# Optimization experiments

Measured on AMD Instinct MI355X. Metric: run time of the kernel, lower is better.

The kernel has to match this reference:

```python
import jax, jax.numpy as jnp
import numpy as np

B, T, C = 4, 2048, 1024
H = 16
D = C // H  # head_dim = 64


def setup_inputs() -> dict:
    key = jax.random.key(0)
    k1, k2, k3 = jax.random.split(key, 3)
    x = jax.random.normal(k1, (B, T, C), dtype=jnp.float32)
    # torch nn.Linear weight layout: [out_features, in_features]; y = x @ W.T
    w_attn = jax.random.normal(k2, (3 * C, C), dtype=jnp.float32) * (1.0 / np.sqrt(C))
    w_proj = jax.random.normal(k3, (C, C), dtype=jnp.float32) * (1.0 / np.sqrt(C))
    return {"x": x, "w_attn": w_attn, "w_proj": w_proj}


def _attention(x, w_attn, w_proj):
    qkv = jnp.einsum('btc,fc->btf', x, w_attn)           # [B,T,3C]
    q, k, v = jnp.split(qkv, 3, axis=-1)
    # [B,T,C] -> [B,H,T,D]
    q = q.reshape(B, T, H, D).transpose(0, 2, 1, 3)
    k = k.reshape(B, T, H, D).transpose(0, 2, 1, 3)
    v = v.reshape(B, T, H, D).transpose(0, 2, 1, 3)
    att = jnp.einsum('bhqd,bhkd->bhqk', q, k) * (1.0 / np.sqrt(D))
    causal = jnp.tril(jnp.ones((T, T), dtype=bool))      # [T,T]
    att = jnp.where(causal[None, None], att, -jnp.inf)
    att = jax.nn.softmax(att, axis=-1)
    out = jnp.einsum('bhqk,bhkd->bhqd', att, v)          # [B,H,T,D]
    out = out.transpose(0, 2, 1, 3).reshape(B, T, C)
    return jnp.einsum('btc,fc->btf', out, w_proj)        # [B,T,C]


def reference(x, w_attn, w_proj):
    return _attention(x, w_attn, w_proj)
```

## Files before the change

kernel.cpp:

```cpp
#include <hip/hip_runtime.h>
#include <hip/hip_bf16.h>

typedef __attribute__((ext_vector_type(8))) short s8b;
typedef __attribute__((ext_vector_type(4))) float f4;
typedef unsigned short u16;

union U8 { s8b v; unsigned long long u[2]; };

__device__ __forceinline__ u16 f2bf(float f) {
  union { float f; unsigned u; } x; x.f = f;
  unsigned r = x.u + 0x7fffu + ((x.u >> 16) & 1u);
  return (u16)(r >> 16);
}

__device__ __forceinline__ float exp2a(float x) {
  float r;
  asm("v_exp_f32 %0, %1" : "=v"(r) : "v"(x));
  return r;
}

__device__ __forceinline__ void gload16(const void* g, void* l) {
  __builtin_amdgcn_global_load_lds(
      (const __attribute__((address_space(1))) void*)g,
      (__attribute__((address_space(3))) void*)l, 16, 0, 0);
}

__global__ void cvt3_kernel(const float* __restrict__ x, const float* __restrict__ wa,
                            const float* __restrict__ wp, u16* __restrict__ xb,
                            u16* __restrict__ wab, u16* __restrict__ wpb) {
  const int i = blockIdx.x * blockDim.x + threadIdx.x;
  const float4* src;
  ushort4* dst;
  int idx;
  if (i < 2097152) { src = (const float4*)x; dst = (ushort4*)xb; idx = i; }
  else if (i < 2883584) { src = (const float4*)wa; dst = (ushort4*)wab; idx = i - 2097152; }
  else { src = (const float4*)wp; dst = (ushort4*)wpb; idx = i - 2883584; }
  const float4 v = src[idx];
  ushort4 o;
  o.x = f2bf(v.x); o.y = f2bf(v.y); o.z = f2bf(v.z); o.w = f2bf(v.w);
  dst[idx] = o;
}

#define BMT 128
#define BNT 128
#define BKT 64

template<int MODE, int TILES>
__global__ __launch_bounds__(256, 2)
void gemm_bt(const u16* __restrict__ A, const u16* __restrict__ Bm,
             float* __restrict__ Cf,
             u16* __restrict__ qo, u16* __restrict__ ko, u16* __restrict__ vo,
             int N, int K, int GX) {
  __shared__ u16 lds[2][2][BMT * BKT];
  const int tid = threadIdx.x;
  const int lane = tid & 63;
  const int w = tid >> 6;
  const int wr = w >> 1, wc = w & 1;
  const int ric = lane >> 3;
  const int ssw = (lane & 7) ^ ric;

  auto tile_ptrs = [&](int t, const u16*& Ab, const u16*& Bb, int& bm, int& bn) {
    const int d = blockIdx.x + t * gridDim.x;
    const int xcd = d & 7, ib = d >> 3;
    bm = xcd * 8 + ib / GX;
    bn = ib % GX;
    Ab = A + (size_t)bm * BMT * K;
    Bb = Bm + (size_t)bn * BNT * K;
  };

  const int nk = K / BKT;
  const u16 *Ab, *Bb, *AbN, *BbN;
  int bm, bn, bmN, bnN;
  tile_ptrs(0, Ab, Bb, bm, bn);

  {
#pragma unroll
    for (int c = 0; c < 4; ++c) {
      const int rch = w * 32 + c * 8;
      gload16(Ab + (size_t)(rch + ric) * K + ssw * 8, &lds[0][0][rch * BKT]);
      gload16(Bb + (size_t)(rch + ric) * K + ssw * 8, &lds[0][1][rch * BKT]);
    }
  }
  __syncthreads();

  for (int t = 0; t < TILES; ++t) {
    if (t + 1 < TILES) tile_ptrs(t + 1, AbN, BbN, bmN, bnN);
    f4 acc[4][4] = {};

    for (int kt = 0; kt < nk; kt += 2) {
#pragma unroll
      for (int h = 0; h < 2; ++h) {
        const int ktg = kt + h;
        {
          const u16* sA;
          const u16* sB;
          int ko_;
          bool do_stage = true;
          if (ktg + 1 < nk) { sA = Ab; sB = Bb; ko_ = (ktg + 1) * BKT; }
          else if (t + 1 < TILES) { sA = AbN; sB = BbN; ko_ = 0; }
          else do_stage = false;
          if (do_stage) {
#pragma unroll
            for (int c = 0; c < 4; ++c) {
              const int rch = w * 32 + c * 8;
              gload16(sA + (size_t)(rch + ric) * K + ko_ + ssw * 8, &lds[h ^ 1][0][rch * BKT]);
              gload16(sB + (size_t)(rch + ric) * K + ko_ + ssw * 8, &lds[h ^ 1][1][rch * BKT]);
            }
          }
        }
        const u16* At = &lds[h][0][0];
        const u16* Bt = &lds[h][1][0];
#pragma unroll
        for (int kk = 0; kk < 2; ++kk) {
          s8b a[4], b[4];
#pragma unroll
          for (int m = 0; m < 4; ++m) {
            const int row = wr * 64 + m * 16 + (lane & 15);
            a[m] = *(const s8b*)(At + row * BKT + ((((kk << 2) + (lane >> 4)) ^ (row & 7)) << 3));
          }
#pragma unroll
          for (int n = 0; n < 4; ++n) {
            const int row = wc * 64 + n * 16 + (lane & 15);
            b[n] = *(const s8b*)(Bt + row * BKT + ((((kk << 2) + (lane >> 4)) ^ (row & 7)) << 3));
          }
#pragma unroll
          for (int m = 0; m < 4; ++m)
#pragma unroll
            for (int n = 0; n < 4; ++n)
              acc[m][n] = __builtin_amdgcn_mfma_f32_16x16x32_bf16(a[m], b[n], acc[m][n], 0, 0, 0);
        }
        __syncthreads();
      }
    }

    if (MODE == 0) {
#pragma unroll
      for (int n = 0; n < 4; ++n) {
        const int f = bn * BNT + wc * 64 + n * 16 + (lane & 15);
        const int which = f >> 10;
        const int rem = f & 1023;
        const int h = rem >> 6, dd = rem & 63;
        if (which == 2) {
#pragma unroll
          for (int m = 0; m < 4; ++m) {
            const int i0 = bm * BMT + wr * 64 + m * 16 + (lane >> 4) * 4;
            const int bb = i0 >> 11, t0 = i0 & 2047;
            ushort4 pk;
            pk.x = f2bf(acc[m][n][0]);
            pk.y = f2bf(acc[m][n][1]);
            pk.z = f2bf(acc[m][n][2]);
            pk.w = f2bf(acc[m][n][3]);
            *(ushort4*)(&vo[((size_t)((bb << 4) + h) * 64 + dd) * 2048 + t0]) = pk;
          }
        } else {
          u16* dst = which == 0 ? qo : ko;
          const float sc = which == 0 ? 0.18033688f : 1.0f;
#pragma unroll
          for (int m = 0; m < 4; ++m) {
#pragma unroll
            for (int j = 0; j < 4; ++j) {
              const int i = bm * BMT + wr * 64 + m * 16 + (lane >> 4) * 4 + j;
              const int bb = i >> 11, tt = i & 2047;
              dst[((size_t)((bb << 4) + h) * 2048 + tt) * 64 + dd] = f2bf(acc[m][n][j] * sc);
            }
          }
        }
      }
    } else {
#pragma unroll
      for (int m = 0; m < 4; ++m) {
#pragma unroll
        for (int j = 0; j < 4; ++j) {
          const int i = bm * BMT + wr * 64 + m * 16 + (lane >> 4) * 4 + j;
#pragma unroll
          for (int n = 0; n < 4; ++n) {
            const int f = bn * BNT + wc * 64 + n * 16 + (lane & 15);
            Cf[(size_t)i * N + f] = acc[m][n][j];
          }
        }
      }
    }

    Ab = AbN; Bb = BbN; bm = bmN; bn = bnN;
  }
}

__global__ __launch_bounds__(256, 3)
void attn_kernel(const u16* __restrict__ q, const u16* __restrict__ k,
                 const u16* __restrict__ vt, u16* __restrict__ ao) {
  __shared__ u16 Kl[2][64 * 64];
  __shared__ u16 VTl[2][64 * 64];
  __shared__ u16 Pl[4][16 * 64];
  const int tid = threadIdx.x, lane = tid & 63, w = tid >> 6;
  const int dd = blockIdx.x;
  const int xcd = dd & 7, ib = dd >> 3;
  const int bh = xcd * 8 + (ib & 7);
  const int j4 = ib >> 3;
  const int s4 = j4 >> 2, r4 = j4 & 3;
  const int qi = (s4 == 0) ? 15 - r4 : (s4 == 1) ? 8 + r4 : (s4 == 2) ? 7 - r4 : r4;
  const int b = bh >> 4, h16 = bh & 15;
  const size_t hb = (size_t)bh * 2048 * 64;
  const int qlo = lane & 15, hi = lane >> 4;
  const int r0 = tid >> 3, sl = tid & 7;
  u16* pw = &Pl[w][0];

  const s8b ones = {16256, 16256, 16256, 16256, 16256, 16256, 16256, 16256};

  const u16* kp = k + hb + (size_t)r0 * 64 + sl * 8;
  const u16* vp = vt + hb + (size_t)r0 * 2048 + sl * 8;
  s8b kr[2], vr[2];
  auto load_regs = [&]() {
    kr[0] = *(const s8b*)kp;
    kr[1] = *(const s8b*)(kp + 32 * 64);
    vr[0] = *(const s8b*)vp;
    vr[1] = *(const s8b*)(vp + 32 * 2048);
    kp += 64 * 64;
    vp += 64;
  };

  auto softpack = [&](f4 (&s)[4], U8 (&pf)[2]) {
#pragma unroll
    for (int n = 0; n < 4; ++n)
#pragma unroll
      for (int j = 0; j < 4; ++j) s[n][j] = exp2a(s[n][j]);
#pragma unroll
    for (int n = 0; n < 4; ++n) {
      __hip_bfloat162 h0 = __float22bfloat162_rn(make_float2(s[n][0], s[n][1]));
      __hip_bfloat162 h1 = __float22bfloat162_rn(make_float2(s[n][2], s[n][3]));
      unsigned lo, hi2;
      __builtin_memcpy(&lo, &h0, 4);
      __builtin_memcpy(&hi2, &h1, 4);
      const unsigned long long w64 =
          (unsigned long long)lo | ((unsigned long long)hi2 << 32);
      const int cw = ((n << 2) + hi) ^ qlo;
      *(unsigned long long*)(pw + (qlo << 6) + (cw << 2)) = w64;
    }
#pragma unroll
    for (int kk = 0; kk < 2; ++kk) {
      const int ca = ((kk << 3) + (hi << 1)) ^ qlo;
      pf[kk].u[0] = *(const unsigned long long*)(pw + (qlo << 6) + (ca << 2));
      pf[kk].u[1] = *(const unsigned long long*)(pw + (qlo << 6) + ((ca ^ 1) << 2));
    }
  };

  const int nkt = 2 * qi + 2;
  s8b qf[2][2];
#pragma unroll
  for (int g = 0; g < 2; ++g) {
    const u16* qp = q + hb + (size_t)(qi * 128 + w * 32 + g * 16 + qlo) * 64 + hi * 8;
    qf[g][0] = *(const s8b*)qp;
    qf[g][1] = *(const s8b*)(qp + 32);
  }
  f4 acc0[5] = {}, acc1[5] = {};

  load_regs();
  {
#pragma unroll
    for (int c0 = 0; c0 < 2; ++c0) {
      const int r = r0 + c0 * 32;
      const int off = r * 64 + ((sl ^ (r & 7) ^ (r >> 3)) << 3);
      *(s8b*)(&Kl[0][off]) = kr[c0];
      *(s8b*)(&VTl[0][off]) = vr[c0];
    }
  }
  __syncthreads();

  for (int kt2 = 0; kt2 < nkt; kt2 += 2) {
#pragma unroll
    for (int h = 0; h < 2; ++h) {
      const int ktg = kt2 + h;
      const bool pf_next = (ktg + 1 < nkt);
      if (pf_next) load_regs();

      f4 s0[4], s1[4];
#pragma unroll
      for (int n = 0; n < 4; ++n) {
        s0[n] = (f4){-64.f, -64.f, -64.f, -64.f};
        s1[n] = (f4){-64.f, -64.f, -64.f, -64.f};
      }
      __builtin_amdgcn_s_setprio(1);
#pragma unroll
      for (int n = 0; n < 4; ++n) {
        const int row = n * 16 + qlo;
        const int swz = (row & 7) ^ (row >> 3);
#pragma unroll
        for (int kk = 0; kk < 2; ++kk) {
          const s8b kf = *(const s8b*)(&Kl[h][row * 64 + ((((kk << 2) + hi) ^ swz) << 3)]);
          s0[n] = __builtin_amdgcn_mfma_f32_16x16x32_bf16(kf, qf[0][kk], s0[n], 0, 0, 0);
          s1[n] = __builtin_amdgcn_mfma_f32_16x16x32_bf16(kf, qf[1][kk], s1[n], 0, 0, 0);
        }
      }
      __builtin_amdgcn_s_setprio(0);

      const int dmb = (2 * qi - ktg) * 64;
      if (dmb < 64) {
        const int thr0 = w * 32 + qlo + dmb;
        const int thr1 = thr0 + 16;
#pragma unroll
        for (int n = 0; n < 4; ++n)
#pragma unroll
          for (int j = 0; j < 4; ++j) {
            const int kidx = n * 16 + hi * 4 + j;
            if (kidx > thr0) s0[n][j] = -1e30f;
            if (kidx > thr1) s1[n][j] = -1e30f;
          }
      }

      U8 pf0[2], pf1[2];
      softpack(s0, pf0);
      softpack(s1, pf1);

      __builtin_amdgcn_s_setprio(1);
#pragma unroll
      for (int dn = 0; dn < 4; ++dn) {
        const int vrow = dn * 16 + qlo;
        const int vswz = (vrow & 7) ^ (vrow >> 3);
#pragma unroll
        for (int kk = 0; kk < 2; ++kk) {
          const s8b vf = *(const s8b*)(&VTl[h][vrow * 64 + ((((kk << 2) + hi) ^ vswz) << 3)]);
          acc0[dn] = __builtin_amdgcn_mfma_f32_16x16x32_bf16(pf0[kk].v, vf, acc0[dn], 0, 0, 0);
          acc1[dn] = __builtin_amdgcn_mfma_f32_16x16x32_bf16(pf1[kk].v, vf, acc1[dn], 0, 0, 0);
        }
      }
#pragma unroll
      for (int kk = 0; kk < 2; ++kk) {
        acc0[4] = __builtin_amdgcn_mfma_f32_16x16x32_bf16(pf0[kk].v, ones, acc0[4], 0, 0, 0);
        acc1[4] = __builtin_amdgcn_mfma_f32_16x16x32_bf16(pf1[kk].v, ones, acc1[4], 0, 0, 0);
      }
      __builtin_amdgcn_s_setprio(0);

      if (pf_next) {
#pragma unroll
        for (int c0 = 0; c0 < 2; ++c0) {
          const int r = r0 + c0 * 32;
          const int off = r * 64 + ((sl ^ (r & 7) ^ (r >> 3)) << 3);
          *(s8b*)(&Kl[h ^ 1][off]) = kr[c0];
          *(s8b*)(&VTl[h ^ 1][off]) = vr[c0];
        }
      }
      __syncthreads();
    }
  }

#pragma unroll
  for (int g = 0; g < 2; ++g) {
    const f4* accg = g ? acc1 : acc0;
#pragma unroll
    for (int j = 0; j < 4; ++j) {
      const float rl = 1.0f / accg[4][j];
      const int t = qi * 128 + w * 32 + g * 16 + hi * 4 + j;
#pragma unroll
      for (int dn = 0; dn < 4; ++dn) {
        const int dcol = dn * 16 + qlo;
        ao[((size_t)(b * 2048 + t)) * 1024 + h16 * 64 + dcol] = f2bf(accg[dn][j] * rl);
      }
    }
  }
}

extern "C" void kernel_launch(void* const* d_in, const int* in_sizes, int n_in,
                              void* d_out, int out_size, void* d_ws, size_t ws_size,
                              hipStream_t stream) {
  const float* x = (const float*)d_in[0];
  const float* w_attn = (const float*)d_in[1];
  const float* w_proj = (const float*)d_in[2];
  float* out = (float*)d_out;
  char* ws = (char*)d_ws;

  u16* xb  = (u16*)(ws);
  u16* wab = (u16*)(ws + (16u << 20));
  u16* wpb = (u16*)(ws + (22u << 20));
  u16* qb  = (u16*)(ws + (24u << 20));
  u16* kb  = (u16*)(ws + (40u << 20));
  u16* vb  = (u16*)(ws + (56u << 20));
  u16* ao  = xb;

  cvt3_kernel<<<12288, 256, 0, stream>>>(x, w_attn, w_proj, xb, wab, wpb);

  gemm_bt<0, 3><<<512, 256, 0, stream>>>(xb, wab, nullptr, qb, kb, vb,
                                         3072, 1024, 24);
  attn_kernel<<<1024, 256, 0, stream>>>(qb, kb, vb, ao);
  gemm_bt<1, 1><<<512, 256, 0, stream>>>(ao, wpb, out, nullptr, nullptr, nullptr,
                                         1024, 1024, 8);
}
```

Measured before the change: 142.0 us.

## Single-buffer K/V tiles in LDS with two barriers per iteration

Replaces the double-buffered K and V^T LDS tiles with a single buffer. The manual two-step unroll becomes a plain loop that waits on a barrier, writes the prefetched registers into LDS, and waits on a second barrier. This halves K/V LDS usage, which may allow more resident blocks per CU. In exchange it adds a second barrier per tile and serialises the LDS store behind the compute of every wave.

```diff
diff --git a/kernel.cpp b/kernel.cpp
--- a/kernel.cpp
+++ b/kernel.cpp
@@ -188,8 +188,8 @@
 __global__ __launch_bounds__(256, 3)
 void attn_kernel(const u16* __restrict__ q, const u16* __restrict__ k,
                  const u16* __restrict__ vt, u16* __restrict__ ao) {
-  __shared__ u16 Kl[2][64 * 64];
-  __shared__ u16 VTl[2][64 * 64];
+  __shared__ u16 Kl[64 * 64];
+  __shared__ u16 VTl[64 * 64];
   __shared__ u16 Pl[4][16 * 64];
   const int tid = threadIdx.x, lane = tid & 63, w = tid >> 6;
   const int dd = blockIdx.x;
@@ -217,6 +217,15 @@
     kp += 64 * 64;
     vp += 64;
   };
+  auto write_lds = [&]() {
+#pragma unroll
+    for (int c0 = 0; c0 < 2; ++c0) {
+      const int r = r0 + c0 * 32;
+      const int off = r * 64 + ((sl ^ (r & 7) ^ (r >> 3)) << 3);
+      *(s8b*)(&Kl[off]) = kr[c0];
+      *(s8b*)(&VTl[off]) = vr[c0];
+    }
+  };
 
   auto softpack = [&](f4 (&s)[4], U8 (&pf)[2]) {
 #pragma unroll
@@ -254,90 +263,73 @@
   f4 acc0[5] = {}, acc1[5] = {};
 
   load_regs();
-  {
-#pragma unroll
-    for (int c0 = 0; c0 < 2; ++c0) {
-      const int r = r0 + c0 * 32;
-      const int off = r * 64 + ((sl ^ (r & 7) ^ (r >> 3)) << 3);
-      *(s8b*)(&Kl[0][off]) = kr[c0];
-      *(s8b*)(&VTl[0][off]) = vr[c0];
-    }
-  }
+  write_lds();
   __syncthreads();
 
-  for (int kt2 = 0; kt2 < nkt; kt2 += 2) {
-#pragma unroll
-    for (int h = 0; h < 2; ++h) {
-      const int ktg = kt2 + h;
-      const bool pf_next = (ktg + 1 < nkt);
-      if (pf_next) load_regs();
-
-      f4 s0[4], s1[4];
-#pragma unroll
-      for (int n = 0; n < 4; ++n) {
-        s0[n] = (f4){-64.f, -64.f, -64.f, -64.f};
-        s1[n] = (f4){-64.f, -64.f, -64.f, -64.f};
-      }
-      __builtin_amdgcn_s_setprio(1);
-#pragma unroll
-      for (int n = 0; n < 4; ++n) {
-        const int row = n * 16 + qlo;
-        const int swz = (row & 7) ^ (row >> 3);
-#pragma unroll
-        for (int kk = 0; kk < 2; ++kk) {
-          const s8b kf = *(const s8b*)(&Kl[h][row * 64 + ((((kk << 2) + hi) ^ swz) << 3)]);
-          s0[n] = __builtin_amdgcn_mfma_f32_16x16x32_bf16(kf, qf[0][kk], s0[n], 0, 0, 0);
-          s1[n] = __builtin_amdgcn_mfma_f32_16x16x32_bf16(kf, qf[1][kk], s1[n], 0, 0, 0);
-        }
-      }
-      __builtin_amdgcn_s_setprio(0);
-
-      const int dmb = (2 * qi - ktg) * 64;
-      if (dmb < 64) {
-        const int thr0 = w * 32 + qlo + dmb;
-        const int thr1 = thr0 + 16;
-#pragma unroll
-        for (int n = 0; n < 4; ++n)
-#pragma unroll
-          for (int j = 0; j < 4; ++j) {
-            const int kidx = n * 16 + hi * 4 + j;
-            if (kidx > thr0) s0[n][j] = -1e30f;
-            if (kidx > thr1) s1[n][j] = -1e30f;
-          }
-      }
-
-      U8 pf0[2], pf1[2];
-      softpack(s0, pf0);
-      softpack(s1, pf1);
-
-      __builtin_amdgcn_s_setprio(1);
-#pragma unroll
-      for (int dn = 0; dn < 4; ++dn) {
-        const int vrow = dn * 16 + qlo;
-        const int vswz = (vrow & 7) ^ (vrow >> 3);
-#pragma unroll
-        for (int kk = 0; kk < 2; ++kk) {
-          const s8b vf = *(const s8b*)(&VTl[h][vrow * 64 + ((((kk << 2) + hi) ^ vswz) << 3)]);
-          acc0[dn] = __builtin_amdgcn_mfma_f32_16x16x32_bf16(pf0[kk].v, vf, acc0[dn], 0, 0, 0);
-          acc1[dn] = __builtin_amdgcn_mfma_f32_16x16x32_bf16(pf1[kk].v, vf, acc1[dn], 0, 0, 0);
-        }
-      }
+  for (int kt = 0; kt < nkt; ++kt) {
+    const bool pf_next = (kt + 1 < nkt);
+    if (pf_next) load_regs();
+
+    f4 s0[4], s1[4];
+#pragma unroll
+    for (int n = 0; n < 4; ++n) {
+      s0[n] = (f4){-64.f, -64.f, -64.f, -64.f};
+      s1[n] = (f4){-64.f, -64.f, -64.f, -64.f};
+    }
+    __builtin_amdgcn_s_setprio(1);
+#pragma unroll
+    for (int n = 0; n < 4; ++n) {
+      const int row = n * 16 + qlo;
+      const int swz = (row & 7) ^ (row >> 3);
 #pragma unroll
       for (int kk = 0; kk < 2; ++kk) {
-        acc0[4] = __builtin_amdgcn_mfma_f32_16x16x32_bf16(pf0[kk].v, ones, acc0[4], 0, 0, 0);
-        acc1[4] = __builtin_amdgcn_mfma_f32_16x16x32_bf16(pf1[kk].v, ones, acc1[4], 0, 0, 0);
-      }
-      __builtin_amdgcn_s_setprio(0);
-
-      if (pf_next) {
-#pragma unroll
-        for (int c0 = 0; c0 < 2; ++c0) {
-          const int r = r0 + c0 * 32;
-          const int off = r * 64 + ((sl ^ (r & 7) ^ (r >> 3)) << 3);
-          *(s8b*)(&Kl[h ^ 1][off]) = kr[c0];
-          *(s8b*)(&VTl[h ^ 1][off]) = vr[c0];
-        }
-      }
+        const s8b kf = *(const s8b*)(&Kl[row * 64 + ((((kk << 2) + hi) ^ swz) << 3)]);
+        s0[n] = __builtin_amdgcn_mfma_f32_16x16x32_bf16(kf, qf[0][kk], s0[n], 0, 0, 0);
+        s1[n] = __builtin_amdgcn_mfma_f32_16x16x32_bf16(kf, qf[1][kk], s1[n], 0, 0, 0);
+      }
+    }
+    __builtin_amdgcn_s_setprio(0);
+
+    const int dmb = (2 * qi - kt) * 64;
+    if (dmb < 64) {
+      const int thr0 = w * 32 + qlo + dmb;
+      const int thr1 = thr0 + 16;
+#pragma unroll
+      for (int n = 0; n < 4; ++n)
+#pragma unroll
+        for (int j = 0; j < 4; ++j) {
+          const int kidx = n * 16 + hi * 4 + j;
+          if (kidx > thr0) s0[n][j] = -1e30f;
+          if (kidx > thr1) s1[n][j] = -1e30f;
+        }
+    }
+
+    U8 pf0[2], pf1[2];
+    softpack(s0, pf0);
+    softpack(s1, pf1);
+
+    __builtin_amdgcn_s_setprio(1);
+#pragma unroll
+    for (int dn = 0; dn < 4; ++dn) {
+      const int vrow = dn * 16 + qlo;
+      const int vswz = (vrow & 7) ^ (vrow >> 3);
+#pragma unroll
+      for (int kk = 0; kk < 2; ++kk) {
+        const s8b vf = *(const s8b*)(&VTl[vrow * 64 + ((((kk << 2) + hi) ^ vswz) << 3)]);
+        acc0[dn] = __builtin_amdgcn_mfma_f32_16x16x32_bf16(pf0[kk].v, vf, acc0[dn], 0, 0, 0);
+        acc1[dn] = __builtin_amdgcn_mfma_f32_16x16x32_bf16(pf1[kk].v, vf, acc1[dn], 0, 0, 0);
+      }
+    }
+#pragma unroll
+    for (int kk = 0; kk < 2; ++kk) {
+      acc0[4] = __builtin_amdgcn_mfma_f32_16x16x32_bf16(pf0[kk].v, ones, acc0[4], 0, 0, 0);
+      acc1[4] = __builtin_amdgcn_mfma_f32_16x16x32_bf16(pf1[kk].v, ones, acc1[4], 0, 0, 0);
+    }
+    __builtin_amdgcn_s_setprio(0);
+
+    __syncthreads();
+    if (pf_next) {
+      write_lds();
       __syncthreads();
     }
   }
```

New measurement: 138.2 us. -2.7%, faster.
